# Kernel tuning notes

Hardware: AMD Instinct MI355X
Metric: run time of the kernel (lower is better)

Reference implementation:

```python
import jax, jax.numpy as jnp
import numpy as np

B, M, E = 8192, 200, 64
OTHER = 128
FEA = 256  # E + E + OTHER
ADIM = 3 * E


def setup_inputs() -> dict:
    key = jax.random.key(0)
    ks = jax.random.split(key, 12)
    s = lambda fan: 1.0 / np.sqrt(fan)
    return {
        "hist": jax.random.normal(ks[0], (B, M, E), jnp.float32),
        "target": jax.random.normal(ks[1], (B, E), jnp.float32),
        "other": jax.random.normal(ks[2], (B, OTHER), jnp.float32),
        "aW1": jax.random.normal(ks[3], (ADIM, ADIM // 2), jnp.float32) * s(ADIM),
        "ab1": jnp.zeros((ADIM // 2,), jnp.float32),
        "aW2": jax.random.normal(ks[4], (ADIM // 2, 1), jnp.float32) * s(ADIM // 2),
        "ab2": jnp.zeros((1,), jnp.float32),
        "oW1": jax.random.normal(ks[5], (FEA, FEA // 2), jnp.float32) * s(FEA),
        "ob1": jnp.zeros((FEA // 2,), jnp.float32),
        "oW2": jax.random.normal(ks[6], (FEA // 2, FEA // 3), jnp.float32) * s(FEA // 2),
        "ob2": jnp.zeros((FEA // 3,), jnp.float32),
        "oW3": jax.random.normal(ks[7], (FEA // 3, FEA // 4), jnp.float32) * s(FEA // 3),
        "ob3": jnp.zeros((FEA // 4,), jnp.float32),
        "fW": jax.random.normal(ks[8], (FEA // 4, 1), jnp.float32) * s(FEA // 4),
        "fb": jnp.zeros((1,), jnp.float32),
    }


def reference(hist, target, other, aW1, ab1, aW2, ab2,
              oW1, ob1, oW2, ob2, oW3, ob3, fW, fb):
    # DIN activation unit, vectorized over the m history steps.
    tgt = target[:, None, :]                                  # [B,1,E]
    a = jnp.concatenate(
        [hist, hist * tgt, jnp.broadcast_to(tgt, hist.shape)], axis=-1
    )                                                          # [B,M,3E]
    h = jax.nn.relu(jnp.einsum("bma,ah->bmh", a, aW1) + ab1)   # [B,M,3E/2]
    aij = jnp.einsum("bmh,ho->bmo", h, aW2) + ab2              # [B,M,1]
    tmp = jnp.sum(aij * hist, axis=1)                          # [B,E]

    x = jnp.concatenate([tmp, target, other], axis=1)          # [B,FEA]
    x = jax.nn.relu(x @ oW1 + ob1)
    x = jax.nn.relu(x @ oW2 + ob2)
    x = jax.nn.relu(x @ oW3 + ob3)
    out = jax.nn.sigmoid(x @ fW + fb)                          # [B,1]
    return out
```

## Files before the change

### kernel.cpp

```cpp
#include <hip/hip_runtime.h>
#include <math.h>

#define BATCH 8192
#define M 200
#define E 64
#define H1 96
#define F1 128
#define F2 85
#define F3 64
#define SH 72
#define MT 13

typedef _Float16 half8_t __attribute__((ext_vector_type(8)));
typedef _Float16 half4_t __attribute__((ext_vector_type(4)));
typedef float floatx4 __attribute__((ext_vector_type(4)));

__global__ __launch_bounds__(256, 3) void din_kernel(
    const float* __restrict__ hist, const float* __restrict__ target,
    const float* __restrict__ other,
    const float* __restrict__ aW1, const float* __restrict__ ab1,
    const float* __restrict__ aW2, const float* __restrict__ ab2,
    const float* __restrict__ oW1, const float* __restrict__ ob1,
    const float* __restrict__ oW2, const float* __restrict__ ob2,
    const float* __restrict__ oW3, const float* __restrict__ ob3,
    const float* __restrict__ fW,  const float* __restrict__ fb,
    float* __restrict__ out)
{
    __shared__ _Float16 histS[208 * SH];
    __shared__ _Float16 WbT[H1 * SH];
    __shared__ float tgtS[E];
    __shared__ float beS[H1];
    __shared__ float aW2S[H1];
    __shared__ float aijS[208];
    __shared__ float partS[4 * E];
    __shared__ float xS[256];
    __shared__ float h1p[256];
    __shared__ float h1S[F1];
    __shared__ float h2p[256];
    __shared__ float h2S[F2];
    __shared__ float h3S[F3];
    __shared__ float ab2S;

    const int t = threadIdx.x;
    const int b = blockIdx.x;

    if (t < E) tgtS[t] = target[(size_t)b * E + t];
    if (t == 0) ab2S = ab2[0];
    __syncthreads();

    for (int idx = t; idx < E * H1; idx += 256) {
        int k = idx / H1, j = idx - k * H1;
        float w = aW1[idx] + tgtS[k] * aW1[E * H1 + idx];
        WbT[j * SH + k] = (_Float16)w;
    }
    if (t < H1) {
        float s = ab1[t];
        for (int k = 0; k < E; ++k)
            s += tgtS[k] * aW1[(2 * E + k) * H1 + t];
        beS[t] = s;
        aW2S[t] = aW2[t];
    }
    {
        const float4* hb4 = (const float4*)(hist + (size_t)b * (M * E));
        for (int i = t; i < (M * E) / 4; i += 256) {
            float4 v = hb4[i];
            int m = i >> 4, c4 = (i & 15) * 4;
            half4_t hv = { (_Float16)v.x, (_Float16)v.y,
                           (_Float16)v.z, (_Float16)v.w };
            *(half4_t*)&histS[m * SH + c4] = hv;
        }
        for (int i = t; i < 8 * 64; i += 256)
            histS[(200 + (i >> 6)) * SH + (i & 63)] = (_Float16)0.f;
    }
    __syncthreads();

    const int lane = t & 63;
    const int wv   = t >> 6;
    const int quad = lane >> 4;
    const int lm   = lane & 15;

    half8_t bf[12];
    #pragma unroll
    for (int nt = 0; nt < 6; ++nt) {
        #pragma unroll
        for (int kk = 0; kk < 2; ++kk)
            bf[nt * 2 + kk] =
                *(const half8_t*)&WbT[(nt * 16 + lm) * SH + kk * 32 + quad * 8];
    }

    for (int mt = wv; mt < MT; mt += 4) {
        const int m0 = mt * 16;
        half8_t a0 = *(const half8_t*)&histS[(m0 + lm) * SH + quad * 8];
        half8_t a1 = *(const half8_t*)&histS[(m0 + lm) * SH + 32 + quad * 8];
        float s0 = 0.f, s1 = 0.f, s2 = 0.f, s3 = 0.f;
        #pragma unroll
        for (int nt = 0; nt < 6; ++nt) {
            floatx4 acc = {0.f, 0.f, 0.f, 0.f};
            acc = __builtin_amdgcn_mfma_f32_16x16x32_f16(a0, bf[nt * 2],     acc, 0, 0, 0);
            acc = __builtin_amdgcn_mfma_f32_16x16x32_f16(a1, bf[nt * 2 + 1], acc, 0, 0, 0);
            float be_n = beS[nt * 16 + lm];
            float w2   = aW2S[nt * 16 + lm];
            s0 += fmaxf(acc[0] + be_n, 0.f) * w2;
            s1 += fmaxf(acc[1] + be_n, 0.f) * w2;
            s2 += fmaxf(acc[2] + be_n, 0.f) * w2;
            s3 += fmaxf(acc[3] + be_n, 0.f) * w2;
        }
        #pragma unroll
        for (int off = 1; off < 16; off <<= 1) {
            s0 += __shfl_xor(s0, off);
            s1 += __shfl_xor(s1, off);
            s2 += __shfl_xor(s2, off);
            s3 += __shfl_xor(s3, off);
        }
        if (lm == 0) {
            int mr = m0 + quad * 4;
            aijS[mr + 0] = s0 + ab2S;
            aijS[mr + 1] = s1 + ab2S;
            aijS[mr + 2] = s2 + ab2S;
            aijS[mr + 3] = s3 + ab2S;
        }
    }
    __syncthreads();

    {
        int k = t & 63, g = t >> 6;
        float s = 0.f;
        for (int m = g * 50; m < g * 50 + 50; ++m)
            s += aijS[m] * (float)histS[m * SH + k];
        partS[g * E + k] = s;
    }
    __syncthreads();

    if (t < 64)
        xS[t] = partS[t] + partS[64 + t] + partS[128 + t] + partS[192 + t];
    else if (t < 128)
        xS[t] = tgtS[t - 64];
    else
        xS[t] = other[(size_t)b * 128 + (t - 128)];
    __syncthreads();

    {
        int j = t & 127, ph = t >> 7;
        float s = ph ? 0.f : ob1[j];
        const float* w = oW1 + (size_t)(ph * 128) * F1 + j;
        int c0 = ph * 128;
        for (int c = 0; c < 128; ++c)
            s += xS[c0 + c] * w[(size_t)c * F1];
        h1p[ph * 128 + j] = s;
    }
    __syncthreads();
    if (t < F1) h1S[t] = fmaxf(h1p[t] + h1p[128 + t], 0.f);
    __syncthreads();

    {
        int o = t & 127, ph = t >> 7;
        if (o < F2) {
            float s = ph ? 0.f : ob2[o];
            int c0 = ph * 64;
            for (int c = c0; c < c0 + 64; ++c)
                s += h1S[c] * oW2[(size_t)c * F2 + o];
            h2p[ph * 128 + o] = s;
        }
    }
    __syncthreads();
    if (t < F2) h2S[t] = fmaxf(h2p[t] + h2p[128 + t], 0.f);
    __syncthreads();

    if (t < F3) {
        float s = ob3[t];
        for (int c = 0; c < F2; ++c)
            s += h2S[c] * oW3[(size_t)c * F3 + t];
        h3S[t] = fmaxf(s, 0.f);
    }
    __syncthreads();

    if (t < 64) {
        float v = h3S[t] * fW[t];
        v += __shfl_xor(v, 1);  v += __shfl_xor(v, 2);  v += __shfl_xor(v, 4);
        v += __shfl_xor(v, 8);  v += __shfl_xor(v, 16); v += __shfl_xor(v, 32);
        if (t == 0) out[b] = 1.f / (1.f + __expf(-(v + fb[0])));
    }
}

extern "C" void kernel_launch(void* const* d_in, const int* in_sizes, int n_in,
                              void* d_out, int out_size, void* d_ws, size_t ws_size,
                              hipStream_t stream) {
    const float* hist   = (const float*)d_in[0];
    const float* target = (const float*)d_in[1];
    const float* other  = (const float*)d_in[2];
    const float* aW1    = (const float*)d_in[3];
    const float* ab1    = (const float*)d_in[4];
    const float* aW2    = (const float*)d_in[5];
    const float* ab2    = (const float*)d_in[6];
    const float* oW1    = (const float*)d_in[7];
    const float* ob1    = (const float*)d_in[8];
    const float* oW2    = (const float*)d_in[9];
    const float* ob2    = (const float*)d_in[10];
    const float* oW3    = (const float*)d_in[11];
    const float* ob3    = (const float*)d_in[12];
    const float* fW     = (const float*)d_in[13];
    const float* fb     = (const float*)d_in[14];
    float* out = (float*)d_out;

    din_kernel<<<BATCH, 256, 0, stream>>>(hist, target, other,
                                          aW1, ab1, aW2, ab2,
                                          oW1, ob1, oW2, ob2, oW3, ob3,
                                          fW, fb, out);
}
```

Baseline: 824.2 us.

## Load history rows straight into MFMA registers and fuse weighted sum in-register

Removes the shared-memory staging of the full history tile. Each wave now loads its rows from global memory directly into fp16 MFMA operands and keeps the fp32 values. The attention-weighted sum is accumulated in registers, using the fp32 history values and the score broadcast by shuffles, then reduced across lanes per wave. This drops about 30KB of LDS, allowing four blocks per CU, and removes one barrier plus a second LDS pass. In exchange the global loads are no longer shared across phases and per-lane loads are strided rather than fully coalesced. It also adds many shuffle reductions and more register pressure.

New measurement: 746.3 us. -9.5%, faster.

```diff
diff --git a/kernel.cpp b/kernel.cpp
--- a/kernel.cpp
+++ b/kernel.cpp
@@ -12,10 +12,9 @@
 #define MT 13
 
 typedef _Float16 half8_t __attribute__((ext_vector_type(8)));
-typedef _Float16 half4_t __attribute__((ext_vector_type(4)));
 typedef float floatx4 __attribute__((ext_vector_type(4)));
 
-__global__ __launch_bounds__(256, 3) void din_kernel(
+__global__ __launch_bounds__(256, 4) void din_kernel(
     const float* __restrict__ hist, const float* __restrict__ target,
     const float* __restrict__ other,
     const float* __restrict__ aW1, const float* __restrict__ ab1,
@@ -26,12 +25,10 @@
     const float* __restrict__ fW,  const float* __restrict__ fb,
     float* __restrict__ out)
 {
-    __shared__ _Float16 histS[208 * SH];
     __shared__ _Float16 WbT[H1 * SH];
     __shared__ float tgtS[E];
     __shared__ float beS[H1];
     __shared__ float aW2S[H1];
-    __shared__ float aijS[208];
     __shared__ float partS[4 * E];
     __shared__ float xS[256];
     __shared__ float h1p[256];
@@ -60,18 +57,6 @@
         beS[t] = s;
         aW2S[t] = aW2[t];
     }
-    {
-        const float4* hb4 = (const float4*)(hist + (size_t)b * (M * E));
-        for (int i = t; i < (M * E) / 4; i += 256) {
-            float4 v = hb4[i];
-            int m = i >> 4, c4 = (i & 15) * 4;
-            half4_t hv = { (_Float16)v.x, (_Float16)v.y,
-                           (_Float16)v.z, (_Float16)v.w };
-            *(half4_t*)&histS[m * SH + c4] = hv;
-        }
-        for (int i = t; i < 8 * 64; i += 256)
-            histS[(200 + (i >> 6)) * SH + (i & 63)] = (_Float16)0.f;
-    }
     __syncthreads();
 
     const int lane = t & 63;
@@ -88,10 +73,25 @@
                 *(const half8_t*)&WbT[(nt * 16 + lm) * SH + kk * 32 + quad * 8];
     }
 
+    float tk0[8], tk1[8];
+    #pragma unroll
+    for (int j = 0; j < 8; ++j) { tk0[j] = 0.f; tk1[j] = 0.f; }
+
+    const int qs16 = (lm >> 2) << 4;
+    const int rsel = lm & 3;
+
     for (int mt = wv; mt < MT; mt += 4) {
         const int m0 = mt * 16;
-        half8_t a0 = *(const half8_t*)&histS[(m0 + lm) * SH + quad * 8];
-        half8_t a1 = *(const half8_t*)&histS[(m0 + lm) * SH + 32 + quad * 8];
+        const int row = m0 + lm;
+        const int rowc = row < M ? row : (M - 1);
+        const float4* p = (const float4*)(hist + ((size_t)b * M + rowc) * E + quad * 8);
+        float4 f0 = p[0], g0 = p[1];
+        float4 f1 = p[8], g1 = p[9];
+        half8_t a0 = { (_Float16)f0.x, (_Float16)f0.y, (_Float16)f0.z, (_Float16)f0.w,
+                       (_Float16)g0.x, (_Float16)g0.y, (_Float16)g0.z, (_Float16)g0.w };
+        half8_t a1 = { (_Float16)f1.x, (_Float16)f1.y, (_Float16)f1.z, (_Float16)f1.w,
+                       (_Float16)g1.x, (_Float16)g1.y, (_Float16)g1.z, (_Float16)g1.w };
+
         float s0 = 0.f, s1 = 0.f, s2 = 0.f, s3 = 0.f;
         #pragma unroll
         for (int nt = 0; nt < 6; ++nt) {
@@ -112,22 +112,36 @@
             s2 += __shfl_xor(s2, off);
             s3 += __shfl_xor(s3, off);
         }
-        if (lm == 0) {
-            int mr = m0 + quad * 4;
-            aijS[mr + 0] = s0 + ab2S;
-            aijS[mr + 1] = s1 + ab2S;
-            aijS[mr + 2] = s2 + ab2S;
-            aijS[mr + 3] = s3 + ab2S;
-        }
-    }
-    __syncthreads();
-
-    {
-        int k = t & 63, g = t >> 6;
-        float s = 0.f;
-        for (int m = g * 50; m < g * 50 + 50; ++m)
-            s += aijS[m] * (float)histS[m * SH + k];
-        partS[g * E + k] = s;
+        float v0 = __shfl(s0, qs16), v1 = __shfl(s1, qs16);
+        float v2 = __shfl(s2, qs16), v3 = __shfl(s3, qs16);
+        float aij = (rsel == 0) ? v0 : (rsel == 1) ? v1 : (rsel == 2) ? v2 : v3;
+        aij += ab2S;
+        aij = (row < M) ? aij : 0.f;
+
+        tk0[0] += f0.x * aij; tk0[1] += f0.y * aij;
+        tk0[2] += f0.z * aij; tk0[3] += f0.w * aij;
+        tk0[4] += g0.x * aij; tk0[5] += g0.y * aij;
+        tk0[6] += g0.z * aij; tk0[7] += g0.w * aij;
+        tk1[0] += f1.x * aij; tk1[1] += f1.y * aij;
+        tk1[2] += f1.z * aij; tk1[3] += f1.w * aij;
+        tk1[4] += g1.x * aij; tk1[5] += g1.y * aij;
+        tk1[6] += g1.z * aij; tk1[7] += g1.w * aij;
+    }
+
+    #pragma unroll
+    for (int j = 0; j < 8; ++j) {
+        #pragma unroll
+        for (int off = 1; off < 16; off <<= 1) {
+            tk0[j] += __shfl_xor(tk0[j], off);
+            tk1[j] += __shfl_xor(tk1[j], off);
+        }
+    }
+    if (lm == 0) {
+        #pragma unroll
+        for (int j = 0; j < 8; ++j) {
+            partS[wv * E + quad * 8 + j]      = tk0[j];
+            partS[wv * E + 32 + quad * 8 + j] = tk1[j];
+        }
     }
     __syncthreads();
 
```
